# Kernel optimization log

Hardware: AMD Instinct MI355X
Metric: run time of the kernel (lower is better)

Reference implementation:

```python
import jax, jax.numpy as jnp
import numpy as np

THRESH = 6.0   # latent_dist_threshold
SCALE = 1.0    # reward_scale
EPS = 1e-6


def _count_scatter(idx, vals):
    # idx, vals: [B, V, N]; counts[b,v,s] = sum of vals over queries whose argmin == s
    B, V, N = idx.shape
    bi = jnp.arange(B)[:, None, None]
    vi = jnp.arange(V)[None, :, None]
    return jnp.zeros((B, V, N), jnp.int32).at[bi, vi, idx].add(vals)


def _direction(min_dists, min_idx, query_xy, source_xy, query_mask):
    # one chamfer direction: queries matched to nearest source particles
    d = jnp.take_along_axis(source_xy, min_idx[..., None], axis=2)  # [B,V,N,2]
    dist = jnp.linalg.norm(query_xy - d, ord=2, axis=-1)            # [B,V,N]
    latent_mask = min_dists > THRESH
    rpm = query_mask | latent_mask                                   # reward_particle_mask
    vals = jnp.where(rpm, 0, 1).astype(jnp.int32)
    count = _count_scatter(min_idx, vals)                            # density counts per source
    w = 1.0 / (jnp.take_along_axis(count, min_idx, axis=2).astype(jnp.float32) + EPS)
    dist = jnp.where(rpm, 0.0, w * dist)
    unmatched = jnp.any((~query_mask) & latent_mask, axis=-1).astype(jnp.float32)
    groups = jnp.maximum(jnp.sum(count > 0, axis=2).astype(jnp.float32) + unmatched, 1.0)
    return -(jnp.sum(dist, axis=2) + unmatched) / groups             # [B,V]


def setup_inputs() -> dict:
    key = jax.random.key(0)
    k1, k2 = jax.random.split(key)
    achieved = jax.random.normal(k1, (256, 2, 512, 10), dtype=jnp.float32)
    desired = jax.random.normal(k2, (256, 2, 512, 10), dtype=jnp.float32)
    return {"achieved": achieved, "desired": desired}


def reference(achieved, desired):
    # latent_classifier=None -> obj_class_cond = ones -> mask = (ones == 0) = all False
    state_mask = jnp.zeros(achieved.shape[:-1], bool)
    goal_mask = jnp.zeros(desired.shape[:-1], bool)
    s_vis = achieved[..., 5:9]
    s_xy = achieved[..., :2]
    g_vis = desired[..., 5:9]
    g_xy = desired[..., :2]
    # 'l2_simple' pairwise squared dist: P[b,v,i,j] = ||s_vis_i - g_vis_j||^2
    P = (jnp.sum(s_vis ** 2, -1)[..., :, None]
         + jnp.sum(g_vis ** 2, -1)[..., None, :]
         - 2.0 * jnp.einsum('bvnd,bvmd->bvnm', s_vis, g_vis))
    P = jnp.where(state_mask[..., :, None] | goal_mask[..., None, :], jnp.inf, P)
    # goal -> state: min over state axis (2)
    md1 = jnp.min(P, axis=2)
    mi1 = jnp.argmin(P, axis=2).astype(jnp.int32)
    r_g2s = _direction(md1, mi1, g_xy, s_xy, goal_mask)
    # state -> goal: min over goal axis (3)
    md2 = jnp.min(P, axis=3)
    mi2 = jnp.argmin(P, axis=3).astype(jnp.int32)
    r_s2g = _direction(md2, mi2, s_xy, g_xy, state_mask)
    rv = (r_g2s + r_s2g) / 2.0                                       # [B,V]
    no_valid = jnp.all(goal_mask, -1) | jnp.all(state_mask, -1)
    rv = jnp.where(no_valid, -1.0, rv)
    reward = jnp.mean(rv, axis=1)
    return SCALE * reward[:, None]                                    # [B,1]
```

## Files before the change

### kernel.cpp

```cpp
#include <hip/hip_runtime.h>
#include <math.h>

#define NB 256
#define NV 2
#define NN 512
#define ND 10
#define THRESH_SQ 6.0f
#define EPS_W 1e-6f

typedef __attribute__((ext_vector_type(8))) short bf16x8;
typedef __attribute__((ext_vector_type(4))) float f32x4;

__device__ __forceinline__ unsigned short f2bf(float x) {
    union { float f; unsigned u; } v; v.f = x;
    unsigned r = v.u + 0x7FFFu + ((v.u >> 16) & 1u);
    return (unsigned short)(r >> 16);
}
__device__ __forceinline__ float bf2f(unsigned short h) {
    union { unsigned u; float f; } v; v.u = ((unsigned)h) << 16; return v.f;
}
__device__ __forceinline__ void split3(float x, unsigned short* s) {
    unsigned short h = f2bf(x); float r = x - bf2f(h);
    unsigned short m = f2bf(r); float r2 = r - bf2f(m);
    s[0] = h; s[1] = m; s[2] = f2bf(r2);
}
__device__ __forceinline__ unsigned umin_(unsigned a, unsigned b) { return a < b ? a : b; }

__device__ __forceinline__ int recaddr(int c, int row) {
    return (c << 13) + ((row << 4) ^ (c << 5));
}

__global__ __launch_bounds__(512, 6)
void chamfer_bv(const float* __restrict__ achieved,
                const float* __restrict__ desired,
                float* __restrict__ rv_out)
{
    const int bv  = blockIdx.x;
    const int tid = threadIdx.x;

    __shared__ __align__(16) char buf[32768];
    __shared__ unsigned colKey[NN];
    __shared__ unsigned rowKeyArr[NN];
    __shared__ int cnt[NN];
    __shared__ float redF[16];
    __shared__ int   redI[16];

    const float* arow = achieved + ((size_t)bv * NN + tid) * ND;
    const float* drow = desired  + ((size_t)bv * NN + tid) * ND;

    const unsigned short ONE = 0x3F80;
    const int pi[6] = {0,0,1,2,1,0};
    const int pj[6] = {0,1,0,0,1,2};

    const float g5 = drow[5], g6 = drow[6], g7 = drow[7], g8 = drow[8];

    {
        float a5 = arow[5], a6 = arow[6], a7 = arow[7], a8 = arow[8];
        unsigned short us[4][3];
        split3(-2.0f*a5, us[0]); split3(-2.0f*a6, us[1]);
        split3(-2.0f*a7, us[2]); split3(-2.0f*a8, us[3]);
        float sn2 = a5*a5 + a6*a6 + a7*a7 + a8*a8;
        unsigned short sn[3]; split3(sn2, sn);
        unsigned short t[32];
        #pragma unroll
        for (int d = 0; d < 4; ++d)
            #pragma unroll
            for (int p = 0; p < 6; ++p)
                t[d*6+p] = us[d][pi[p]];
        t[24]=sn[0]; t[25]=sn[1]; t[26]=sn[2];
        t[27]=ONE;   t[28]=ONE;   t[29]=ONE;
        t[30]=ONE;   t[31]=0;
        #pragma unroll
        for (int c = 0; c < 4; ++c) {
            bf16x8 v;
            #pragma unroll
            for (int e = 0; e < 8; ++e) v[e] = (short)t[c*8+e];
            *(bf16x8*)(buf + recaddr(c, tid)) = v;
        }
    }
    colKey[tid] = 0xFFFFFFFFu;
    cnt[tid] = 0;
    __syncthreads();

    const int lane = tid & 63, wid = tid >> 6;
    const int lrow = lane & 15, lchk = lane >> 4;

    bf16x8 afr[4];
    #pragma unroll
    for (int nt = 0; nt < 4; ++nt)
        afr[nt] = *(const bf16x8*)(buf + recaddr(lchk, (wid<<6) + (nt<<4) + lrow));
    __syncthreads();

    {
        unsigned short gs[4][3];
        split3(g5, gs[0]); split3(g6, gs[1]); split3(g7, gs[2]); split3(g8, gs[3]);
        float gn2 = g5*g5 + g6*g6 + g7*g7 + g8*g8;
        unsigned short gn[3]; split3(gn2, gn);
        unsigned short t[32];
        #pragma unroll
        for (int d = 0; d < 4; ++d)
            #pragma unroll
            for (int p = 0; p < 6; ++p)
                t[d*6+p] = gs[d][pj[p]];
        t[24]=ONE;   t[25]=ONE;   t[26]=ONE;
        t[27]=gn[0]; t[28]=gn[1]; t[29]=gn[2];
        t[30]=0x3A80; t[31]=0;
        #pragma unroll
        for (int c = 0; c < 4; ++c) {
            bf16x8 v;
            #pragma unroll
            for (int e = 0; e < 8; ++e) v[e] = (short)t[c*8+e];
            *(bf16x8*)(buf + recaddr(c, tid)) = v;
        }
    }
    __syncthreads();

    unsigned rowKey[4][4];
    int ncst[4][4];
    #pragma unroll
    for (int nt = 0; nt < 4; ++nt)
        #pragma unroll
        for (int j = 0; j < 4; ++j) {
            rowKey[nt][j] = 0xFFFFFFFFu;
            ncst[nt][j]   = (wid<<6) + (nt<<4) + (lchk<<2) + j;
        }

    const unsigned MASK = 0xFFFFFE00u;
    const f32x4 z = {0.0f, 0.0f, 0.0f, 0.0f};

    #pragma unroll 4
    for (int mt = 0; mt < 32; ++mt) {
        bf16x8 bfr = *(const bf16x8*)(buf + recaddr(lchk, (mt<<4) + lrow));
        const unsigned mcur = (unsigned)((mt<<4) + lrow);
        unsigned cv = 0xFFFFFFFFu;
        #pragma unroll
        for (int nt = 0; nt < 4; ++nt) {
            f32x4 acc = __builtin_amdgcn_mfma_f32_16x16x32_bf16(afr[nt], bfr, z, 0, 0, 0);
            #pragma unroll
            for (int j = 0; j < 4; ++j) {
                unsigned bits = __float_as_uint(acc[j]);
                unsigned kr = (bits & MASK) | mcur;
                unsigned kc = (bits & MASK) | (unsigned)ncst[nt][j];
                rowKey[nt][j] = umin_(rowKey[nt][j], kr);
                cv = umin_(cv, kc);
            }
        }
        atomicMin(&colKey[mcur], cv);
    }

    #pragma unroll
    for (int nt = 0; nt < 4; ++nt) {
        #pragma unroll
        for (int j = 0; j < 4; ++j) {
            unsigned v = rowKey[nt][j];
            #pragma unroll
            for (int s = 1; s <= 8; s <<= 1)
                v = umin_(v, (unsigned)__shfl_xor((int)v, s));
            if (lrow == 0) rowKeyArr[ncst[nt][j]] = v;
        }
    }
    __syncthreads();

    const unsigned kA = colKey[tid];
    const unsigned kB = rowKeyArr[tid];
    const int miA = (int)(kA & 0x1FFu);
    const int miB = (int)(kB & 0x1FFu);
    const bool latA = __uint_as_float(kA & MASK) > THRESH_SQ;
    const bool latB = __uint_as_float(kB & MASK) > THRESH_SQ;
    if (!latA) atomicAdd(&cnt[miA], 1);
    if (!latB) atomicAdd(&cnt[miB], 0x10000);
    __syncthreads();

    float sumA = 0.0f, sumB = 0.0f;
    if (!latA) {
        const float* sp = achieved + ((size_t)bv * NN + miA) * ND;
        float dx = drow[0] - sp[0], dy = drow[1] - sp[1];
        float w = 1.0f / ((float)(cnt[miA] & 0xFFFF) + EPS_W);
        sumA = w * sqrtf(dx*dx + dy*dy);
    }
    if (!latB) {
        const float* gp = desired + ((size_t)bv * NN + miB) * ND;
        float dx = arow[0] - gp[0], dy = arow[1] - gp[1];
        float w = 1.0f / ((float)(((unsigned)cnt[miB]) >> 16) + EPS_W);
        sumB = w * sqrtf(dx*dx + dy*dy);
    }
    const int c0 = cnt[tid];
    int grpPk = ((c0 & 0xFFFF) ? 1 : 0) | ((((unsigned)c0) >> 16) ? 0x10000 : 0);
    int latPk = (latA ? 1 : 0) | (latB ? 2 : 0);

    #pragma unroll
    for (int off = 32; off > 0; off >>= 1) {
        sumA  += __shfl_down(sumA, off);
        sumB  += __shfl_down(sumB, off);
        grpPk += __shfl_down(grpPk, off);
        latPk |= __shfl_down(latPk, off);
    }
    if (lane == 0) {
        redF[wid*2] = sumA; redF[wid*2+1] = sumB;
        redI[wid*2] = grpPk; redI[wid*2+1] = latPk;
    }
    __syncthreads();
    if (tid == 0) {
        float sA = 0.0f, sB = 0.0f; int G = 0, L = 0;
        #pragma unroll
        for (int w2 = 0; w2 < 8; ++w2) {
            sA += redF[w2*2]; sB += redF[w2*2+1];
            G  += redI[w2*2]; L |= redI[w2*2+1];
        }
        float unmA = (L & 1) ? 1.0f : 0.0f;
        float unmB = (L & 2) ? 1.0f : 0.0f;
        float gA = (float)(G & 0xFFFF), gB = (float)(((unsigned)G) >> 16);
        float rA = -(sA + unmA) / fmaxf(gA + unmA, 1.0f);
        float rB = -(sB + unmB) / fmaxf(gB + unmB, 1.0f);
        rv_out[bv] = 0.5f * (rA + rB);
    }
}

__global__ void chamfer_finalize(const float* __restrict__ rv, float* __restrict__ out)
{
    int b = blockIdx.x * 256 + threadIdx.x;
    if (b < NB) out[b] = 0.5f * (rv[2*b] + rv[2*b + 1]);
}

extern "C" void kernel_launch(void* const* d_in, const int* in_sizes, int n_in,
                              void* d_out, int out_size, void* d_ws, size_t ws_size,
                              hipStream_t stream)
{
    const float* achieved = (const float*)d_in[0];
    const float* desired  = (const float*)d_in[1];
    float* out = (float*)d_out;
    float* rv  = (float*)d_ws;

    chamfer_bv<<<NB * NV, 512, 0, stream>>>(achieved, desired, rv);
    chamfer_finalize<<<1, 256, 0, stream>>>(rv, out);
}
```

Baseline: 32.04 us.

## Alias post-GEMM scratch into staging buffer, split colKey atomics, raise occupancy

Reuses the bf16 staging buffer for rowKeyArr, cnt and reduction scratch after the MFMA loop, cutting static LDS use, and raises launch_bounds min blocks from 6 to 8 per CU. The column-min atomics are split into two slices per column, indexed by lane chunk, so fewer lanes contend on each address; the slices are merged later. Rowkey shuffles are finished before the barrier and stored afterwards. The tighter register budget risks spills, and the column slot array doubles in size.

```diff
diff --git a/kernel.cpp b/kernel.cpp
--- a/kernel.cpp
+++ b/kernel.cpp
@@ -30,7 +30,7 @@
     return (c << 13) + ((row << 4) ^ (c << 5));
 }
 
-__global__ __launch_bounds__(512, 6)
+__global__ __launch_bounds__(512, 8)
 void chamfer_bv(const float* __restrict__ achieved,
                 const float* __restrict__ desired,
                 float* __restrict__ rv_out)
@@ -39,11 +39,7 @@
     const int tid = threadIdx.x;
 
     __shared__ __align__(16) char buf[32768];
-    __shared__ unsigned colKey[NN];
-    __shared__ unsigned rowKeyArr[NN];
-    __shared__ int cnt[NN];
-    __shared__ float redF[16];
-    __shared__ int   redI[16];
+    __shared__ unsigned colKey[NN * 2];
 
     const float* arow = achieved + ((size_t)bv * NN + tid) * ND;
     const float* drow = desired  + ((size_t)bv * NN + tid) * ND;
@@ -78,8 +74,8 @@
             *(bf16x8*)(buf + recaddr(c, tid)) = v;
         }
     }
-    colKey[tid] = 0xFFFFFFFFu;
-    cnt[tid] = 0;
+    colKey[tid*2]   = 0xFFFFFFFFu;
+    colKey[tid*2+1] = 0xFFFFFFFFu;
     __syncthreads();
 
     const int lane = tid & 63, wid = tid >> 6;
@@ -127,6 +123,7 @@
 
     const unsigned MASK = 0xFFFFFE00u;
     const f32x4 z = {0.0f, 0.0f, 0.0f, 0.0f};
+    const int cslice = lchk >> 1;
 
     #pragma unroll 4
     for (int mt = 0; mt < 32; ++mt) {
@@ -139,13 +136,11 @@
             #pragma unroll
             for (int j = 0; j < 4; ++j) {
                 unsigned bits = __float_as_uint(acc[j]);
-                unsigned kr = (bits & MASK) | mcur;
-                unsigned kc = (bits & MASK) | (unsigned)ncst[nt][j];
-                rowKey[nt][j] = umin_(rowKey[nt][j], kr);
-                cv = umin_(cv, kc);
+                rowKey[nt][j] = umin_(rowKey[nt][j], (bits & MASK) | mcur);
+                cv = umin_(cv, (bits & MASK) | (unsigned)ncst[nt][j]);
             }
         }
-        atomicMin(&colKey[mcur], cv);
+        atomicMin(&colKey[(mcur << 1) | cslice], cv);
     }
 
     #pragma unroll
@@ -156,12 +151,27 @@
             #pragma unroll
             for (int s = 1; s <= 8; s <<= 1)
                 v = umin_(v, (unsigned)__shfl_xor((int)v, s));
-            if (lrow == 0) rowKeyArr[ncst[nt][j]] = v;
-        }
-    }
-    __syncthreads();
-
-    const unsigned kA = colKey[tid];
+            rowKey[nt][j] = v;
+        }
+    }
+    __syncthreads();
+
+    unsigned* rowKeyArr = (unsigned*)buf;
+    int*      cnt       = (int*)(buf + 2048);
+    float*    redF      = (float*)(buf + 4096);
+    int*      redI      = (int*)(buf + 4160);
+
+    if (lrow == 0) {
+        #pragma unroll
+        for (int nt = 0; nt < 4; ++nt)
+            #pragma unroll
+            for (int j = 0; j < 4; ++j)
+                rowKeyArr[ncst[nt][j]] = rowKey[nt][j];
+    }
+    cnt[tid] = 0;
+    __syncthreads();
+
+    const unsigned kA = umin_(colKey[tid*2], colKey[tid*2+1]);
     const unsigned kB = rowKeyArr[tid];
     const int miA = (int)(kA & 0x1FFu);
     const int miB = (int)(kB & 0x1FFu);
```

Measured after the change: 112.1 us. +249.9%, slower.
